# Performance work log

Hardware: AMD Instinct MI355X
Metric: run time of the kernel (lower is better)

## Reference

```python
import jax, jax.numpy as jnp
import numpy as np

KNN = 5
MAX_STEPS = 100
LAM = 1.0  # bound_lambda


def setup_inputs() -> dict:
    key = jax.random.key(0)
    k1, k2 = jax.random.split(key)
    # probabilities in (0,1): softmax-like scores
    scores_raw = jax.random.uniform(k1, (1, 8192, 8, 8), dtype=jnp.float32)
    feats = jax.random.normal(k2, (1, 8192, 256, 1, 1), dtype=jnp.float32)
    return {"scores_raw": scores_raw, "feats": feats}


def knn_affinity(X, knn):
    # X: (N, D) L2-normalized features. Same math as torch.norm(x_i - x_j):
    # ||xi-xj|| = sqrt(|xi|^2 + |xj|^2 - 2 xi.xj), avoids the O(N^2 D) broadcast.
    N = X.shape[0]
    sq = jnp.sum(X * X, axis=-1)                                  # (N,)
    dist2 = sq[:, None] + sq[None, :] - 2.0 * (X @ X.T)           # (N, N)
    dist = jnp.sqrt(jnp.maximum(dist2, 0.0))
    n_neighbors = min(knn + 1, N)
    _, idx = jax.lax.top_k(-dist, n_neighbors)                    # smallest distances
    idx = idx[:, 1:]                                              # drop self
    W = jnp.zeros((N, N), X.dtype).at[jnp.arange(N)[:, None], idx].set(1.0)
    return W


def reference(scores_raw, feats):
    _, _, H, W = scores_raw.shape
    unary = -jnp.log(scores_raw.reshape(-1, H * W) + 1e-10)       # (N, K)
    f = feats.reshape(feats.shape[0], feats.shape[1], -1)[0]       # (N, D), flatten(-3).squeeze(0)
    nrm = jnp.linalg.norm(f, axis=-1, keepdims=True)
    f = f / jnp.maximum(nrm, 1e-12)                                # F.normalize(p=2)
    kernel = knn_affinity(f, KNN)                                  # (N, N)

    Y0 = jax.nn.softmax(-unary, axis=-1)

    def cond(state):
        i, Y, oldE, conv = state
        return (i < MAX_STEPS) & (~conv)

    def body(state):
        i, Y, oldE, _ = state
        pairwise = LAM * (kernel @ Y)                              # (N, K)
        Ynew = jax.nn.softmax(-unary + pairwise, axis=-1)
        # entropy_energy (note: lambda multiplies pairwise again, as in source)
        E = jnp.sum(unary * Ynew - LAM * pairwise * Ynew
                    + Ynew * jnp.log(jnp.clip(Ynew, 1e-20)))
        conv = (i > 1) & (jnp.abs(E - oldE) <= 1e-8 * jnp.abs(oldE))
        return (i + 1, Ynew, E, conv)

    init = (jnp.int32(0), Y0, jnp.float32(jnp.inf), jnp.bool_(False))
    _, Y, _, _ = jax.lax.while_loop(cond, body, init)
    return Y
```

## Files before the change

### kernel.cpp

```cpp
#include <hip/hip_runtime.h>
#include <math.h>

#define NROWS 8192
#define DIM   256
#define NCLS  64
#define KNN   5
#define NCAND 8
#define NSPLIT 4
#define MAXSTEPS 100
#define PBLK 256

struct GS {
  double Eold;
  double Epart[PBLK];
  int pad0[30];
  int gcnt[16 * 32];
  int root; int pad1[31];
  int gen;  int pad2[31];
  int flag; int pad3[31];
};

typedef __attribute__((ext_vector_type(8))) short bf16x8;
typedef __attribute__((ext_vector_type(4))) float f32x4;

typedef __attribute__((address_space(1))) unsigned int glb_u32_t;
typedef __attribute__((address_space(3))) unsigned int lds_u32_t;
__device__ __forceinline__ void async_cp16(const uint4* g, uint4* l) {
  __builtin_amdgcn_global_load_lds((const glb_u32_t*)(const unsigned int*)g,
                                   (lds_u32_t*)(unsigned int*)l, 16, 0, 0);
}

__device__ __forceinline__ float aloadf(const float* p) {
  return __hip_atomic_load(p, __ATOMIC_RELAXED, __HIP_MEMORY_SCOPE_AGENT);
}
__device__ __forceinline__ void astoref(float* p, float v) {
  __hip_atomic_store(p, v, __ATOMIC_RELAXED, __HIP_MEMORY_SCOPE_AGENT);
}
__device__ __forceinline__ double aloadd(const double* p) {
  return __hip_atomic_load(p, __ATOMIC_RELAXED, __HIP_MEMORY_SCOPE_AGENT);
}
__device__ __forceinline__ void astored(double* p, double v) {
  __hip_atomic_store(p, v, __ATOMIC_RELAXED, __HIP_MEMORY_SCOPE_AGENT);
}
__device__ __forceinline__ int aloadi(const int* p) {
  return __hip_atomic_load(p, __ATOMIC_RELAXED, __HIP_MEMORY_SCOPE_AGENT);
}
__device__ __forceinline__ void astorei(int* p, int v) {
  __hip_atomic_store(p, v, __ATOMIC_RELAXED, __HIP_MEMORY_SCOPE_AGENT);
}
__device__ __forceinline__ int afetchadd(int* p) {
  return __hip_atomic_fetch_add(p, 1, __ATOMIC_RELAXED, __HIP_MEMORY_SCOPE_AGENT);
}

__device__ __forceinline__ float wave_sum64(float v) {
#pragma unroll
  for (int m = 32; m >= 1; m >>= 1) v += __shfl_xor(v, m, 64);
  return v;
}
__device__ __forceinline__ double wave_sum64d(double v) {
#pragma unroll
  for (int m = 32; m >= 1; m >>= 1) v += __shfl_xor(v, m, 64);
  return v;
}

__device__ __forceinline__ unsigned short f2bf(float x) {
  unsigned u = __float_as_uint(x);
  u += 0x7FFFu + ((u >> 16) & 1u);
  return (unsigned short)(u >> 16);
}

__device__ __forceinline__ void cs_desc(unsigned& a, unsigned& b) {
  unsigned hi = a > b ? a : b;
  unsigned lo = a > b ? b : a;
  a = hi; b = lo;
}

__global__ void k_normalize(const float* __restrict__ feats, uint2* __restrict__ fb2,
                            float* __restrict__ f, double* __restrict__ sqd) {
  int row  = blockIdx.x * 4 + (threadIdx.x >> 6);
  int lane = threadIdx.x & 63;
  float4 v = ((const float4*)(feats + (size_t)row * DIM))[lane];
  double ss = (double)v.x * v.x + (double)v.y * v.y + (double)v.z * v.z + (double)v.w * v.w;
  ss = wave_sum64d(ss);
  float nr = fmaxf((float)sqrt(ss), 1e-12f);
  float4 o;
  o.x = v.x / nr; o.y = v.y / nr; o.z = v.z / nr; o.w = v.w / nr;
  ((float4*)(f + (size_t)row * DIM))[lane] = o;
  double s2 = (double)o.x * o.x + (double)o.y * o.y + (double)o.z * o.z + (double)o.w * o.w;
  s2 = wave_sum64d(s2);
  if (lane == 0) sqd[row] = s2;
  uint2 w2;
  w2.x = (unsigned)f2bf(o.x) | ((unsigned)f2bf(o.y) << 16);
  w2.y = (unsigned)f2bf(o.z) | ((unsigned)f2bf(o.w) << 16);
  int T = row >> 6, rl = row & 63, g = lane >> 1, h = lane & 1;
  fb2[((size_t)T * 2048 + rl * 32 + (g ^ (rl & 31))) * 2 + h] = w2;
}

#define JSPAN (NROWS / NSPLIT)
#define GTILES (JSPAN / 64)

__launch_bounds__(256, 2)
__global__ void k_gram(const uint4* __restrict__ fb, int* __restrict__ candp) {
  __shared__ uint4 Bsh4[2][2048];
  __shared__ unsigned Ksh[4096];

  const int t  = threadIdx.x;
  const int ib = blockIdx.x >> 2;
  const int js = blockIdx.x & 3;
  const int i0 = ib * 64;
  const int jbase = js * JSPAN;
  const int w = t >> 6, lane = t & 63;

  {
    const uint4* At = fb + (size_t)ib * 2048;
    const uint4* Bt = fb + (size_t)(js * 32) * 2048;
#pragma unroll
    for (int p = 0; p < 8; ++p) {
      int c = w * 8 + p;
      async_cp16(At + c * 64 + lane, &Bsh4[1][c * 64]);
      async_cp16(Bt + c * 64 + lane, &Bsh4[0][c * 64]);
    }
  }
  const int ahalf = w >> 1, bhalf = w & 1;
  const int m15 = lane & 15, quad = lane >> 4;

  __syncthreads();

  bf16x8 areg[2][8];
#pragma unroll
  for (int s = 0; s < 2; ++s) {
    int ra = ahalf * 32 + s * 16 + m15;
#pragma unroll
    for (int kc = 0; kc < 8; ++kc)
      areg[s][kc] = ((const bf16x8*)Bsh4[1])[ra * 32 + ((kc * 4 + quad) ^ (ra & 31))];
  }
  __syncthreads();

  unsigned mk[2][NCAND];
#pragma unroll
  for (int s = 0; s < 2; ++s)
#pragma unroll
    for (int k = 0; k < NCAND; ++k) mk[s][k] = 0u;
  float thr[2] = {-1e30f, -1e30f};

  for (int jt = 0; jt < GTILES; ++jt) {
    const int cbuf = jt & 1;
    if (jt > 0) __syncthreads();
    if (jt + 1 < GTILES) {
      const uint4* Bt = fb + (size_t)(js * 32 + jt + 1) * 2048;
#pragma unroll
      for (int p = 0; p < 8; ++p) {
        int c = w * 8 + p;
        async_cp16(Bt + c * 64 + lane, &Bsh4[1 - cbuf][c * 64]);
      }
    }

    f32x4 acc[2][2];
#pragma unroll
    for (int si = 0; si < 2; ++si)
#pragma unroll
      for (int s = 0; s < 2; ++s) acc[si][s] = (f32x4)(0.f);

#pragma unroll
    for (int kc = 0; kc < 8; ++kc) {
      bf16x8 bv[2];
#pragma unroll
      for (int si = 0; si < 2; ++si) {
        int rb = bhalf * 32 + si * 16 + m15;
        bv[si] = ((const bf16x8*)Bsh4[cbuf])[rb * 32 + ((kc * 4 + quad) ^ (rb & 31))];
      }
      acc[0][0] = __builtin_amdgcn_mfma_f32_16x16x32_bf16(bv[0], areg[0][kc], acc[0][0], 0, 0, 0);
      acc[0][1] = __builtin_amdgcn_mfma_f32_16x16x32_bf16(bv[0], areg[1][kc], acc[0][1], 0, 0, 0);
      acc[1][0] = __builtin_amdgcn_mfma_f32_16x16x32_bf16(bv[1], areg[0][kc], acc[1][0], 0, 0, 0);
      acc[1][1] = __builtin_amdgcn_mfma_f32_16x16x32_bf16(bv[1], areg[1][kc], acc[1][1], 0, 0, 0);
    }

    {
      const unsigned cbase = (unsigned)(jt * 64 + bhalf * 32 + quad * 4);
#pragma unroll
      for (int s = 0; s < 2; ++s) {
        f32x4 v0 = acc[0][s], v1 = acc[1][s];
        float g0 = fmaxf(fmaxf(v0[0], v0[1]), fmaxf(v0[2], v0[3]));
        float g1 = fmaxf(fmaxf(v1[0], v1[1]), fmaxf(v1[2], v1[3]));
        if (fmaxf(g0, g1) > thr[s]) {
          unsigned n[8];
#pragma unroll
          for (int e = 0; e < 4; ++e) {
            unsigned ub0 = __float_as_uint(v0[e]);
            n[e] = ((ub0 ^ (unsigned)(((int)ub0 >> 31) | 0x80000000)) & ~2047u)
                   | (cbase + (unsigned)e);
            unsigned ub1 = __float_as_uint(v1[e]);
            n[4 + e] = ((ub1 ^ (unsigned)(((int)ub1 >> 31) | 0x80000000)) & ~2047u)
                       | (cbase + 16u + (unsigned)e);
          }
          cs_desc(n[0], n[1]); cs_desc(n[2], n[3]); cs_desc(n[4], n[5]); cs_desc(n[6], n[7]);
          cs_desc(n[0], n[2]); cs_desc(n[1], n[3]); cs_desc(n[4], n[6]); cs_desc(n[5], n[7]);
          cs_desc(n[1], n[2]); cs_desc(n[5], n[6]);
          cs_desc(n[0], n[4]); cs_desc(n[1], n[5]); cs_desc(n[2], n[6]); cs_desc(n[3], n[7]);
          cs_desc(n[2], n[4]); cs_desc(n[3], n[5]);
          cs_desc(n[1], n[2]); cs_desc(n[3], n[4]); cs_desc(n[5], n[6]);
          unsigned m[8];
#pragma unroll
          for (int i = 0; i < 8; ++i)
            m[i] = mk[s][i] > n[7 - i] ? mk[s][i] : n[7 - i];
          cs_desc(m[0], m[4]); cs_desc(m[1], m[5]); cs_desc(m[2], m[6]); cs_desc(m[3], m[7]);
          cs_desc(m[0], m[2]); cs_desc(m[1], m[3]); cs_desc(m[4], m[6]); cs_desc(m[5], m[7]);
          cs_desc(m[0], m[1]); cs_desc(m[2], m[3]); cs_desc(m[4], m[5]); cs_desc(m[6], m[7]);
#pragma unroll
          for (int i = 0; i < 8; ++i) mk[s][i] = m[i];
          unsigned kb = mk[s][NCAND - 1] & ~2047u;
          if (kb) {
            unsigned xm = 0x80000000u | ~(unsigned)((int)kb >> 31);
            thr[s] = __uint_as_float(kb ^ xm);
          }
        }
      }
    }
  }

  __syncthreads();
#pragma unroll
  for (int s = 0; s < 2; ++s) {
    int row = ahalf * 32 + s * 16 + m15;
    int slot0 = bhalf * 32 + quad * 8;
#pragma unroll
    for (int k = 0; k < NCAND; ++k)
      Ksh[row * 64 + ((slot0 + k + row) & 63)] = mk[s][k];
  }
  __syncthreads();
  if (t < 64) {
    unsigned fk[NCAND];
#pragma unroll
    for (int k = 0; k < NCAND; ++k) fk[k] = 0u;
    for (int s = 0; s < 64; ++s) {
      unsigned kk = Ksh[t * 64 + ((s + t) & 63)];
      if (kk > fk[NCAND - 1]) {
        fk[NCAND - 1] = kk;
#pragma unroll
        for (int q = NCAND - 1; q >= 1; --q)
          if (fk[q] > fk[q - 1]) { unsigned tm = fk[q]; fk[q] = fk[q - 1]; fk[q - 1] = tm; }
      }
    }
#pragma unroll
    for (int k = 0; k < NCAND; ++k)
      candp[(size_t)js * (NROWS * NCAND) + (size_t)(i0 + t) * NCAND + k] =
          jbase + (int)(fk[k] & 2047u);
  }
}

__global__ void k_refine(const float* __restrict__ f, const double* __restrict__ sqd,
                         const int* __restrict__ candp, int* __restrict__ nbr) {
  const int row = blockIdx.x * 4 + (threadIdx.x >> 6);
  const int t = threadIdx.x & 63;
  const int c = t >> 1;
  const int seg = t & 1;
  const int split = c >> 3, slot = c & 7;
  int j = candp[(size_t)split * (NROWS * NCAND) + (size_t)row * NCAND + slot];
  const float4* fi4 = (const float4*)(f + (size_t)row * DIM) + seg * 32;
  const float4* fj4 = (const float4*)(f + (size_t)j * DIM) + seg * 32;
  double dot = 0.0;
#pragma unroll 8
  for (int d4 = 0; d4 < 32; ++d4) {
    float4 a = fi4[d4], b = fj4[d4];
    dot = fma((double)a.x, (double)b.x, dot);
    dot = fma((double)a.y, (double)b.y, dot);
    dot = fma((double)a.z, (double)b.z, dot);
    dot = fma((double)a.w, (double)b.w, dot);
  }
  dot += __shfl_xor(dot, 1, 64);
  double key = sqd[j] - 2.0 * dot;
  bool valid = (seg == 0) && (j != row);
  for (int s = 0; s < KNN; ++s) {
    double v = valid ? key : (double)INFINITY;
    int vj = valid ? j : 0x7fffffff;
#pragma unroll
    for (int m = 1; m < 64; m <<= 1) {
      double ov = __shfl_xor(v, m, 64);
      int oj = __shfl_xor(vj, m, 64);
      if (ov < v || (ov == v && oj < vj)) { v = ov; vj = oj; }
    }
    if (valid && vj == j) valid = false;
    if (t == 0) nbr[(size_t)row * 8 + s] = vj;
  }
}

__global__ void k_solve(const float* __restrict__ scores,
                        const int* __restrict__ nbr,
                        float* __restrict__ Ya, float* __restrict__ Yb,
                        float* __restrict__ out, GS* __restrict__ gs) {
  const int b = blockIdx.x;
  const int w = threadIdx.x >> 6, lane = threadIdx.x & 63;
  const int row0 = b * 32 + w * 4;
  const int grp = (b & 15) * 32;
  __shared__ int nbl[32][5];
  __shared__ double sE[8];
  __shared__ int sflag;

  if (threadIdx.x < 160)
    nbl[threadIdx.x / 5][threadIdx.x % 5] =
        nbr[(size_t)(b * 32 + threadIdx.x / 5) * 8 + (threadIdx.x % 5)];

  float u[4], y[4];
#pragma unroll
  for (int r = 0; r < 4; ++r)
    u[r] = -logf(scores[(size_t)(row0 + r) * NCLS + lane] + 1e-10f);
#pragma unroll
  for (int r = 0; r < 4; ++r) {
    float e = expf(-u[r]);
    float sum = wave_sum64(e);
    y[r] = e / sum;
    astoref(&Ya[(size_t)(row0 + r) * NCLS + lane], y[r]);
  }
  __syncthreads();

  int nboff[4][KNN];
#pragma unroll
  for (int r = 0; r < 4; ++r)
#pragma unroll
    for (int k = 0; k < KNN; ++k)
      nboff[r][k] = nbl[w * 4 + r][k] * NCLS + lane;

  int mygen = 1;
  if (threadIdx.x == 0) {
    __builtin_amdgcn_fence(__ATOMIC_RELEASE, "workgroup");
    int old = afetchadd(&gs->gcnt[grp]);
    if (old == 15) {
      int r = afetchadd(&gs->root);
      if (r == 15) {
#pragma unroll
        for (int m = 0; m < 16; ++m) astorei(&gs->gcnt[m * 32], 0);
        astorei(&gs->root, 0);
        __builtin_amdgcn_fence(__ATOMIC_RELEASE, "workgroup");
        astorei(&gs->gen, mygen);
      }
    }
    while (aloadi(&gs->gen) < mygen) __builtin_amdgcn_s_sleep(1);
  }
  __syncthreads();
  ++mygen;

  for (int iter = 0; iter < MAXSTEPS; ++iter) {
    const float* __restrict__ Yin = (iter & 1) ? Yb : Ya;
    float* __restrict__ Yout = (iter & 1) ? Ya : Yb;
    double ew = 0.0;
#pragma unroll
    for (int r = 0; r < 4; ++r) {
      float pw = 0.f;
#pragma unroll
      for (int k = 0; k < KNN; ++k) pw += aloadf(&Yin[nboff[r][k]]);
      float e = expf(pw - u[r]);
      float sum = wave_sum64(e);
      y[r] = e / sum;
      astoref(&Yout[(size_t)(row0 + r) * NCLS + lane], y[r]);
      ew += -(double)logf(sum);
    }
    if (lane == 0) sE[w] = ew;
    __syncthreads();
    if (w == 0) {
      double be = (lane < 8) ? sE[lane] : 0.0;
      be = wave_sum64d(be);
      int last = 0;
      if (lane == 0) {
        astored(&gs->Epart[b], be);
        __builtin_amdgcn_fence(__ATOMIC_RELEASE, "workgroup");
        int old = afetchadd(&gs->gcnt[grp]);
        if (old == 15) {
          int r = afetchadd(&gs->root);
          last = (r == 15);
        }
      }
      last = __shfl(last, 0, 64);
      if (last) {
        double s = 0.0;
#pragma unroll
        for (int i = 0; i < 4; ++i) s += aloadd(&gs->Epart[lane + 64 * i]);
        s = wave_sum64d(s);
        if (lane < 16) astorei(&gs->gcnt[lane * 32], 0);
        if (lane == 0) {
          astorei(&gs->root, 0);
          double eo = aloadd(&gs->Eold);
          int conv = (iter > 1) && (fabs(s - eo) <= 1e-8 * fabs(eo));
          astorei(&gs->flag, conv);
          if (!conv) astored(&gs->Eold, s);
        }
        __builtin_amdgcn_fence(__ATOMIC_RELEASE, "workgroup");
        if (lane == 0) astorei(&gs->gen, mygen);
      }
      if (lane == 0) {
        while (aloadi(&gs->gen) < mygen) __builtin_amdgcn_s_sleep(1);
        sflag = aloadi(&gs->flag);
      }
    }
    __syncthreads();
    ++mygen;
    if (sflag) break;
  }

#pragma unroll
  for (int r = 0; r < 4; ++r)
    out[(size_t)(row0 + r) * NCLS + lane] = y[r];
}

__global__ void k_init(GS* gs) {
  int t = threadIdx.x;
  if (t == 0) {
    gs->Eold = (double)INFINITY;
    gs->root = 0; gs->gen = 0; gs->flag = 0;
  }
  if (t < 16 * 32) gs->gcnt[t] = 0;
}

extern "C" void kernel_launch(void* const* d_in, const int* in_sizes, int n_in,
                              void* d_out, int out_size, void* d_ws, size_t ws_size,
                              hipStream_t stream) {
  (void)in_sizes; (void)n_in; (void)out_size; (void)ws_size;
  const float* scores = (const float*)d_in[0];
  const float* feats  = (const float*)d_in[1];
  float* out = (float*)d_out;
  char* ws = (char*)d_ws;
  uint4*  fb    = (uint4*)(ws + 0);
  float*  f     = (float*)(ws + 4194304);
  float*  Ya    = (float*)(ws + 4194304);
  float*  Yb    = (float*)(ws + 6291456);
  double* sqd   = (double*)(ws + 12582912);
  int*    candp = (int*)(ws + 12648448);
  int*    nbr   = (int*)(ws + 13697024);
  GS*     gs    = (GS*)(ws + 13959168);

  k_init<<<1, 512, 0, stream>>>(gs);
  k_normalize<<<NROWS / 4, 256, 0, stream>>>(feats, (uint2*)fb, f, sqd);
  k_gram<<<(NROWS / 64) * NSPLIT, 256, 0, stream>>>(fb, candp);
  k_refine<<<NROWS / 4, 256, 0, stream>>>(f, sqd, candp, nbr);
  k_solve<<<PBLK, 512, 0, stream>>>(scores, nbr, Ya, Yb, out, gs);
}
```

Baseline: 227.0 us.

## Shrink gram tiles to 32x32 per block with one MFMA per wave

The gram/top-k kernel now processes 32-row A tiles against 32-column B tiles, with each wave owning a single 16x16 output fragment. This halves shared memory per block, reuses the B buffer for the candidate-merge scratch, raises launch bounds to 4 blocks per CU, and doubles the grid. Block indices are remapped so that blocks sharing a B span are spread out. The aim is higher occupancy and more blocks to fill the GPU, at the cost of less data reuse per load (more global/LDS traffic per MFMA) and more per-tile top-k merge overhead.

```diff
diff --git a/kernel.cpp b/kernel.cpp
--- a/kernel.cpp
+++ b/kernel.cpp
@@ -97,143 +97,121 @@
 }
 
 #define JSPAN (NROWS / NSPLIT)
-#define GTILES (JSPAN / 64)
-
-__launch_bounds__(256, 2)
+#define GT2 (JSPAN / 32)
+
+__launch_bounds__(256, 4)
 __global__ void k_gram(const uint4* __restrict__ fb, int* __restrict__ candp) {
-  __shared__ uint4 Bsh4[2][2048];
-  __shared__ unsigned Ksh[4096];
-
-  const int t  = threadIdx.x;
-  const int ib = blockIdx.x >> 2;
-  const int js = blockIdx.x & 3;
-  const int i0 = ib * 64;
+  __shared__ uint4 Bsh4[2][1024];
+
+  const int t = threadIdx.x;
+  const int L   = (blockIdx.x & 7) * 128 + (blockIdx.x >> 3);
+  const int js  = L >> 8;
+  const int ib2 = L & 255;
+  const int i0 = ib2 * 32;
   const int jbase = js * JSPAN;
   const int w = t >> 6, lane = t & 63;
+  const int s = w & 1, si = w >> 1;
+  const int m15 = lane & 15, quad = lane >> 4;
+
+  const size_t abase = (size_t)(ib2 >> 1) * 2048 + (size_t)(ib2 & 1) * 1024;
 
   {
-    const uint4* At = fb + (size_t)ib * 2048;
+    const uint4* At = fb + abase;
     const uint4* Bt = fb + (size_t)(js * 32) * 2048;
 #pragma unroll
-    for (int p = 0; p < 8; ++p) {
-      int c = w * 8 + p;
+    for (int p = 0; p < 4; ++p) {
+      int c = w * 4 + p;
       async_cp16(At + c * 64 + lane, &Bsh4[1][c * 64]);
       async_cp16(Bt + c * 64 + lane, &Bsh4[0][c * 64]);
     }
   }
-  const int ahalf = w >> 1, bhalf = w & 1;
-  const int m15 = lane & 15, quad = lane >> 4;
-
-  __syncthreads();
-
-  bf16x8 areg[2][8];
-#pragma unroll
-  for (int s = 0; s < 2; ++s) {
-    int ra = ahalf * 32 + s * 16 + m15;
+  __syncthreads();
+
+  bf16x8 areg[8];
+  {
+    int lr = s * 16 + m15;
 #pragma unroll
     for (int kc = 0; kc < 8; ++kc)
-      areg[s][kc] = ((const bf16x8*)Bsh4[1])[ra * 32 + ((kc * 4 + quad) ^ (ra & 31))];
-  }
-  __syncthreads();
-
-  unsigned mk[2][NCAND];
-#pragma unroll
-  for (int s = 0; s < 2; ++s)
-#pragma unroll
-    for (int k = 0; k < NCAND; ++k) mk[s][k] = 0u;
-  float thr[2] = {-1e30f, -1e30f};
-
-  for (int jt = 0; jt < GTILES; ++jt) {
+      areg[kc] = ((const bf16x8*)Bsh4[1])[lr * 32 + ((kc * 4 + quad) ^ (lr & 31))];
+  }
+  __syncthreads();
+
+  unsigned mk[NCAND];
+#pragma unroll
+  for (int k = 0; k < NCAND; ++k) mk[k] = 0u;
+  float thr = -1e30f;
+
+  for (int jt = 0; jt < GT2; ++jt) {
     const int cbuf = jt & 1;
     if (jt > 0) __syncthreads();
-    if (jt + 1 < GTILES) {
-      const uint4* Bt = fb + (size_t)(js * 32 + jt + 1) * 2048;
-#pragma unroll
-      for (int p = 0; p < 8; ++p) {
-        int c = w * 8 + p;
+    if (jt + 1 < GT2) {
+      const int jn = jt + 1;
+      const uint4* Bt = fb + (size_t)(js * 32 + (jn >> 1)) * 2048 + (size_t)(jn & 1) * 1024;
+#pragma unroll
+      for (int p = 0; p < 4; ++p) {
+        int c = w * 4 + p;
         async_cp16(Bt + c * 64 + lane, &Bsh4[1 - cbuf][c * 64]);
       }
     }
 
-    f32x4 acc[2][2];
-#pragma unroll
-    for (int si = 0; si < 2; ++si)
-#pragma unroll
-      for (int s = 0; s < 2; ++s) acc[si][s] = (f32x4)(0.f);
-
+    f32x4 acc = (f32x4)(0.f);
 #pragma unroll
     for (int kc = 0; kc < 8; ++kc) {
-      bf16x8 bv[2];
-#pragma unroll
-      for (int si = 0; si < 2; ++si) {
-        int rb = bhalf * 32 + si * 16 + m15;
-        bv[si] = ((const bf16x8*)Bsh4[cbuf])[rb * 32 + ((kc * 4 + quad) ^ (rb & 31))];
-      }
-      acc[0][0] = __builtin_amdgcn_mfma_f32_16x16x32_bf16(bv[0], areg[0][kc], acc[0][0], 0, 0, 0);
-      acc[0][1] = __builtin_amdgcn_mfma_f32_16x16x32_bf16(bv[0], areg[1][kc], acc[0][1], 0, 0, 0);
-      acc[1][0] = __builtin_amdgcn_mfma_f32_16x16x32_bf16(bv[1], areg[0][kc], acc[1][0], 0, 0, 0);
-      acc[1][1] = __builtin_amdgcn_mfma_f32_16x16x32_bf16(bv[1], areg[1][kc], acc[1][1], 0, 0, 0);
+      int rb = si * 16 + m15;
+      bf16x8 bv = ((const bf16x8*)Bsh4[cbuf])[rb * 32 + ((kc * 4 + quad) ^ (rb & 31))];
+      acc = __builtin_amdgcn_mfma_f32_16x16x32_bf16(bv, areg[kc], acc, 0, 0, 0);
     }
 
     {
-      const unsigned cbase = (unsigned)(jt * 64 + bhalf * 32 + quad * 4);
-#pragma unroll
-      for (int s = 0; s < 2; ++s) {
-        f32x4 v0 = acc[0][s], v1 = acc[1][s];
-        float g0 = fmaxf(fmaxf(v0[0], v0[1]), fmaxf(v0[2], v0[3]));
-        float g1 = fmaxf(fmaxf(v1[0], v1[1]), fmaxf(v1[2], v1[3]));
-        if (fmaxf(g0, g1) > thr[s]) {
-          unsigned n[8];
-#pragma unroll
-          for (int e = 0; e < 4; ++e) {
-            unsigned ub0 = __float_as_uint(v0[e]);
-            n[e] = ((ub0 ^ (unsigned)(((int)ub0 >> 31) | 0x80000000)) & ~2047u)
-                   | (cbase + (unsigned)e);
-            unsigned ub1 = __float_as_uint(v1[e]);
-            n[4 + e] = ((ub1 ^ (unsigned)(((int)ub1 >> 31) | 0x80000000)) & ~2047u)
-                       | (cbase + 16u + (unsigned)e);
-          }
-          cs_desc(n[0], n[1]); cs_desc(n[2], n[3]); cs_desc(n[4], n[5]); cs_desc(n[6], n[7]);
-          cs_desc(n[0], n[2]); cs_desc(n[1], n[3]); cs_desc(n[4], n[6]); cs_desc(n[5], n[7]);
-          cs_desc(n[1], n[2]); cs_desc(n[5], n[6]);
-          cs_desc(n[0], n[4]); cs_desc(n[1], n[5]); cs_desc(n[2], n[6]); cs_desc(n[3], n[7]);
-          cs_desc(n[2], n[4]); cs_desc(n[3], n[5]);
-          cs_desc(n[1], n[2]); cs_desc(n[3], n[4]); cs_desc(n[5], n[6]);
-          unsigned m[8];
-#pragma unroll
-          for (int i = 0; i < 8; ++i)
-            m[i] = mk[s][i] > n[7 - i] ? mk[s][i] : n[7 - i];
-          cs_desc(m[0], m[4]); cs_desc(m[1], m[5]); cs_desc(m[2], m[6]); cs_desc(m[3], m[7]);
-          cs_desc(m[0], m[2]); cs_desc(m[1], m[3]); cs_desc(m[4], m[6]); cs_desc(m[5], m[7]);
-          cs_desc(m[0], m[1]); cs_desc(m[2], m[3]); cs_desc(m[4], m[5]); cs_desc(m[6], m[7]);
-#pragma unroll
-          for (int i = 0; i < 8; ++i) mk[s][i] = m[i];
-          unsigned kb = mk[s][NCAND - 1] & ~2047u;
-          if (kb) {
-            unsigned xm = 0x80000000u | ~(unsigned)((int)kb >> 31);
-            thr[s] = __uint_as_float(kb ^ xm);
-          }
+      float g4 = fmaxf(fmaxf(acc[0], acc[1]), fmaxf(acc[2], acc[3]));
+      if (g4 > thr) {
+        const unsigned cbase = (unsigned)(jt * 32 + si * 16 + quad * 4);
+        unsigned n[4];
+#pragma unroll
+        for (int e = 0; e < 4; ++e) {
+          unsigned ub = __float_as_uint(acc[e]);
+          n[e] = ((ub ^ (unsigned)(((int)ub >> 31) | 0x80000000)) & ~2047u)
+                 | (cbase + (unsigned)e);
         }
-      }
-    }
-  }
-
-  __syncthreads();
-#pragma unroll
-  for (int s = 0; s < 2; ++s) {
-    int row = ahalf * 32 + s * 16 + m15;
-    int slot0 = bhalf * 32 + quad * 8;
+        cs_desc(n[0], n[1]); cs_desc(n[2], n[3]);
+        cs_desc(n[0], n[2]); cs_desc(n[1], n[3]);
+        cs_desc(n[1], n[2]);
+        unsigned m[8];
+        m[0] = mk[0]; m[1] = mk[1]; m[2] = mk[2]; m[3] = mk[3];
+        m[4] = mk[4] > n[3] ? mk[4] : n[3];
+        m[5] = mk[5] > n[2] ? mk[5] : n[2];
+        m[6] = mk[6] > n[1] ? mk[6] : n[1];
+        m[7] = mk[7] > n[0] ? mk[7] : n[0];
+        cs_desc(m[0], m[4]); cs_desc(m[1], m[5]); cs_desc(m[2], m[6]); cs_desc(m[3], m[7]);
+        cs_desc(m[0], m[2]); cs_desc(m[1], m[3]); cs_desc(m[4], m[6]); cs_desc(m[5], m[7]);
+        cs_desc(m[0], m[1]); cs_desc(m[2], m[3]); cs_desc(m[4], m[5]); cs_desc(m[6], m[7]);
+#pragma unroll
+        for (int i = 0; i < 8; ++i) mk[i] = m[i];
+        unsigned kb = mk[NCAND - 1] & ~2047u;
+        if (kb) {
+          unsigned xm = 0x80000000u | ~(unsigned)((int)kb >> 31);
+          thr = __uint_as_float(kb ^ xm);
+        }
+      }
+    }
+  }
+
+  __syncthreads();
+  unsigned* Ksh = (unsigned*)Bsh4;
+  {
+    int row = s * 16 + m15;
+    int slot0 = (si * 4 + quad) * 8;
 #pragma unroll
     for (int k = 0; k < NCAND; ++k)
-      Ksh[row * 64 + ((slot0 + k + row) & 63)] = mk[s][k];
-  }
-  __syncthreads();
-  if (t < 64) {
+      Ksh[row * 64 + ((slot0 + k + row) & 63)] = mk[k];
+  }
+  __syncthreads();
+  if (t < 32) {
     unsigned fk[NCAND];
 #pragma unroll
     for (int k = 0; k < NCAND; ++k) fk[k] = 0u;
-    for (int s = 0; s < 64; ++s) {
-      unsigned kk = Ksh[t * 64 + ((s + t) & 63)];
+    for (int ss = 0; ss < 64; ++ss) {
+      unsigned kk = Ksh[t * 64 + ((ss + t) & 63)];
       if (kk > fk[NCAND - 1]) {
         fk[NCAND - 1] = kk;
 #pragma unroll
@@ -429,7 +407,7 @@
 
   k_init<<<1, 512, 0, stream>>>(gs);
   k_normalize<<<NROWS / 4, 256, 0, stream>>>(feats, (uint2*)fb, f, sqd);
-  k_gram<<<(NROWS / 64) * NSPLIT, 256, 0, stream>>>(fb, candp);
+  k_gram<<<(NROWS / 32) * NSPLIT, 256, 0, stream>>>(fb, candp);
   k_refine<<<NROWS / 4, 256, 0, stream>>>(f, sqd, candp, nbr);
   k_solve<<<PBLK, 512, 0, stream>>>(scores, nbr, Ya, Yb, out, gs);
 }
```

Measured after the change: 235.8 us. +3.9%, slower.
